# Kernel optimization log

Hardware: AMD Instinct MI355X
Metric: run time of the kernel (lower is better)

## Reference

```python
import jax, jax.numpy as jnp
import numpy as np

L, B = 64, 7          # n_layers, n_bit_options
EPS = 0.02            # sinkhorn entropic regularizer
ITERS = 200           # sinkhorn iterations
TINY = 1e-40


def setup_inputs() -> dict:
    key = jax.random.key(0)
    k1, k2, k3, k4 = jax.random.split(key, 4)
    theta = jax.random.normal(k1, (L, B), dtype=jnp.float32)
    phi = jax.random.normal(k2, (B,), dtype=jnp.float32)
    # layer sizes (param counts), positive; matches layer_sizes buffer usage
    n = jax.random.uniform(k3, (L,), dtype=jnp.float32, minval=4096.0, maxval=262144.0)
    sens = jax.random.uniform(k4, (L,), dtype=jnp.float32)
    sens = sens / sens.sum()  # update_sensitivity normalizes to a distribution
    bits = jnp.arange(2, 2 + B, dtype=jnp.float32)
    err = 2.0 ** (-2.0 * bits)  # quantization error per bitwidth
    return {"theta": theta, "phi": phi, "n": n, "sens": sens, "err": err}


def reference(theta, phi, n, sens, err):
    # DiffAllocator.compute_P
    a = n / n.sum()                         # row marginal (buffer 'a')
    b = jax.nn.softmax(phi)                 # col marginal b()
    C = (n * sens)[:, None] * err[None, :]  # build_cost: [L,B]
    K = -(C - theta) / EPS                  # log-kernel
    log_a = jnp.log(a + TINY)
    log_b = jnp.log(b + TINY)
    f0 = jnp.zeros((L,), dtype=theta.dtype)
    g0 = jnp.zeros((B,), dtype=theta.dtype)

    def step(carry, _):
        f, g = carry
        f = log_a - jax.scipy.special.logsumexp(K + g[None, :], axis=1)
        g = log_b - jax.scipy.special.logsumexp(K + f[:, None], axis=0)
        return (f, g), None

    (f, g), _ = jax.lax.scan(step, (f0, g0), None, length=ITERS)
    P = jnp.exp(K + f[:, None] + g[None, :])
    return P / (P.sum() + TINY)
```

## Files before the change

kernel.cpp:

```cpp
#include <hip/hip_runtime.h>
#include <math.h>

#define NB 7
#define EPS_ 0.02f
#define ITERS1_ 120
#define ITERS2_ 80
#define TINY_ 1e-40f
#define LOG2E_ 1.4426950408889634f
#define LN2_   0.6931471805599453f

__device__ __forceinline__ float exp2_hw(float x) {
#if __has_builtin(__builtin_amdgcn_exp2f)
    return __builtin_amdgcn_exp2f(x);
#else
    return __expf(x * LN2_);
#endif
}
__device__ __forceinline__ float log2_hw(float x) {
#if __has_builtin(__builtin_amdgcn_logf)
    return __builtin_amdgcn_logf(x);
#else
    return __logf(x) * LOG2E_;
#endif
}
__device__ __forceinline__ float rcp_hw(float x) {
#if __has_builtin(__builtin_amdgcn_rcpf)
    return __builtin_amdgcn_rcpf(x);
#else
    return 1.0f / x;
#endif
}

template <int CTRL>
__device__ __forceinline__ float dpp_ident(float identity, float x) {
    return __int_as_float(__builtin_amdgcn_update_dpp(
        __float_as_int(identity), __float_as_int(x), CTRL, 0xF, 0xF, false));
}
__device__ __forceinline__ float readlane63(float x) {
    return __int_as_float(__builtin_amdgcn_readlane(__float_as_int(x), 63));
}
__device__ __forceinline__ float wave_sum_bcast(float s) {
    s += dpp_ident<0x111>(0.f, s);
    s += dpp_ident<0x112>(0.f, s);
    s += dpp_ident<0x114>(0.f, s);
    s += dpp_ident<0x118>(0.f, s);
    s += dpp_ident<0x142>(0.f, s);
    s += dpp_ident<0x143>(0.f, s);
    return readlane63(s);
}

#define WAVE_MAX7(v0,v1,v2,v3,v4,v5,v6, m0,m1,m2,m3,m4,m5,m6)                 \
  {                                                                           \
    float r0,r1,r2,r3,r4,r5,r6;                                               \
    asm("v_mov_b32 %0, %14\n\t"                                               \
        "v_mov_b32 %1, %15\n\t"                                               \
        "v_mov_b32 %2, %16\n\t"                                               \
        "v_mov_b32 %3, %17\n\t"                                               \
        "v_mov_b32 %4, %18\n\t"                                               \
        "v_mov_b32 %5, %19\n\t"                                               \
        "v_mov_b32 %6, %20\n\t"                                               \
        "v_max_f32_dpp %0, %0, %0 row_shr:1 row_mask:0xf bank_mask:0xf\n\t"   \
        "v_max_f32_dpp %1, %1, %1 row_shr:1 row_mask:0xf bank_mask:0xf\n\t"   \
        "v_max_f32_dpp %2, %2, %2 row_shr:1 row_mask:0xf bank_mask:0xf\n\t"   \
        "v_max_f32_dpp %3, %3, %3 row_shr:1 row_mask:0xf bank_mask:0xf\n\t"   \
        "v_max_f32_dpp %4, %4, %4 row_shr:1 row_mask:0xf bank_mask:0xf\n\t"   \
        "v_max_f32_dpp %5, %5, %5 row_shr:1 row_mask:0xf bank_mask:0xf\n\t"   \
        "v_max_f32_dpp %6, %6, %6 row_shr:1 row_mask:0xf bank_mask:0xf\n\t"   \
        "v_max_f32_dpp %0, %0, %0 row_shr:2 row_mask:0xf bank_mask:0xf\n\t"   \
        "v_max_f32_dpp %1, %1, %1 row_shr:2 row_mask:0xf bank_mask:0xf\n\t"   \
        "v_max_f32_dpp %2, %2, %2 row_shr:2 row_mask:0xf bank_mask:0xf\n\t"   \
        "v_max_f32_dpp %3, %3, %3 row_shr:2 row_mask:0xf bank_mask:0xf\n\t"   \
        "v_max_f32_dpp %4, %4, %4 row_shr:2 row_mask:0xf bank_mask:0xf\n\t"   \
        "v_max_f32_dpp %5, %5, %5 row_shr:2 row_mask:0xf bank_mask:0xf\n\t"   \
        "v_max_f32_dpp %6, %6, %6 row_shr:2 row_mask:0xf bank_mask:0xf\n\t"   \
        "v_max_f32_dpp %0, %0, %0 row_shr:4 row_mask:0xf bank_mask:0xf\n\t"   \
        "v_max_f32_dpp %1, %1, %1 row_shr:4 row_mask:0xf bank_mask:0xf\n\t"   \
        "v_max_f32_dpp %2, %2, %2 row_shr:4 row_mask:0xf bank_mask:0xf\n\t"   \
        "v_max_f32_dpp %3, %3, %3 row_shr:4 row_mask:0xf bank_mask:0xf\n\t"   \
        "v_max_f32_dpp %4, %4, %4 row_shr:4 row_mask:0xf bank_mask:0xf\n\t"   \
        "v_max_f32_dpp %5, %5, %5 row_shr:4 row_mask:0xf bank_mask:0xf\n\t"   \
        "v_max_f32_dpp %6, %6, %6 row_shr:4 row_mask:0xf bank_mask:0xf\n\t"   \
        "v_max_f32_dpp %0, %0, %0 row_shr:8 row_mask:0xf bank_mask:0xf\n\t"   \
        "v_max_f32_dpp %1, %1, %1 row_shr:8 row_mask:0xf bank_mask:0xf\n\t"   \
        "v_max_f32_dpp %2, %2, %2 row_shr:8 row_mask:0xf bank_mask:0xf\n\t"   \
        "v_max_f32_dpp %3, %3, %3 row_shr:8 row_mask:0xf bank_mask:0xf\n\t"   \
        "v_max_f32_dpp %4, %4, %4 row_shr:8 row_mask:0xf bank_mask:0xf\n\t"   \
        "v_max_f32_dpp %5, %5, %5 row_shr:8 row_mask:0xf bank_mask:0xf\n\t"   \
        "v_max_f32_dpp %6, %6, %6 row_shr:8 row_mask:0xf bank_mask:0xf\n\t"   \
        "v_max_f32_dpp %0, %0, %0 row_bcast:15 row_mask:0xa bank_mask:0xf\n\t"\
        "v_max_f32_dpp %1, %1, %1 row_bcast:15 row_mask:0xa bank_mask:0xf\n\t"\
        "v_max_f32_dpp %2, %2, %2 row_bcast:15 row_mask:0xa bank_mask:0xf\n\t"\
        "v_max_f32_dpp %3, %3, %3 row_bcast:15 row_mask:0xa bank_mask:0xf\n\t"\
        "v_max_f32_dpp %4, %4, %4 row_bcast:15 row_mask:0xa bank_mask:0xf\n\t"\
        "v_max_f32_dpp %5, %5, %5 row_bcast:15 row_mask:0xa bank_mask:0xf\n\t"\
        "v_max_f32_dpp %6, %6, %6 row_bcast:15 row_mask:0xa bank_mask:0xf\n\t"\
        "v_max_f32_dpp %0, %0, %0 row_bcast:31 row_mask:0xc bank_mask:0xf\n\t"\
        "v_max_f32_dpp %1, %1, %1 row_bcast:31 row_mask:0xc bank_mask:0xf\n\t"\
        "v_max_f32_dpp %2, %2, %2 row_bcast:31 row_mask:0xc bank_mask:0xf\n\t"\
        "v_max_f32_dpp %3, %3, %3 row_bcast:31 row_mask:0xc bank_mask:0xf\n\t"\
        "v_max_f32_dpp %4, %4, %4 row_bcast:31 row_mask:0xc bank_mask:0xf\n\t"\
        "v_max_f32_dpp %5, %5, %5 row_bcast:31 row_mask:0xc bank_mask:0xf\n\t"\
        "v_max_f32_dpp %6, %6, %6 row_bcast:31 row_mask:0xc bank_mask:0xf\n\t"\
        "v_readlane_b32 %7, %0, 63\n\t"                                       \
        "v_readlane_b32 %8, %1, 63\n\t"                                       \
        "v_readlane_b32 %9, %2, 63\n\t"                                       \
        "v_readlane_b32 %10, %3, 63\n\t"                                      \
        "v_readlane_b32 %11, %4, 63\n\t"                                      \
        "v_readlane_b32 %12, %5, 63\n\t"                                      \
        "v_readlane_b32 %13, %6, 63\n\t"                                      \
        "s_nop 1"                                                             \
        : "=&v"(r0), "=&v"(r1), "=&v"(r2), "=&v"(r3),                         \
          "=&v"(r4), "=&v"(r5), "=&v"(r6),                                    \
          "=s"(m0), "=s"(m1), "=s"(m2), "=s"(m3),                             \
          "=s"(m4), "=s"(m5), "=s"(m6)                                        \
        : "v"(v0), "v"(v1), "v"(v2), "v"(v3), "v"(v4), "v"(v5), "v"(v6));     \
  }

#define WAVE_SUM7(e0,e1,e2,e3,e4,e5,e6, s0_,s1_,s2_,s3_,s4_,s5_,s6_)          \
    asm("s_nop 1\n\t"                                                         \
        "v_add_f32_dpp %0, %0, %0 row_shr:1 row_mask:0xf bank_mask:0xf\n\t"   \
        "v_add_f32_dpp %1, %1, %1 row_shr:1 row_mask:0xf bank_mask:0xf\n\t"   \
        "v_add_f32_dpp %2, %2, %2 row_shr:1 row_mask:0xf bank_mask:0xf\n\t"   \
        "v_add_f32_dpp %3, %3, %3 row_shr:1 row_mask:0xf bank_mask:0xf\n\t"   \
        "v_add_f32_dpp %4, %4, %4 row_shr:1 row_mask:0xf bank_mask:0xf\n\t"   \
        "v_add_f32_dpp %5, %5, %5 row_shr:1 row_mask:0xf bank_mask:0xf\n\t"   \
        "v_add_f32_dpp %6, %6, %6 row_shr:1 row_mask:0xf bank_mask:0xf\n\t"   \
        "v_add_f32_dpp %0, %0, %0 row_shr:2 row_mask:0xf bank_mask:0xf\n\t"   \
        "v_add_f32_dpp %1, %1, %1 row_shr:2 row_mask:0xf bank_mask:0xf\n\t"   \
        "v_add_f32_dpp %2, %2, %2 row_shr:2 row_mask:0xf bank_mask:0xf\n\t"   \
        "v_add_f32_dpp %3, %3, %3 row_shr:2 row_mask:0xf bank_mask:0xf\n\t"   \
        "v_add_f32_dpp %4, %4, %4 row_shr:2 row_mask:0xf bank_mask:0xf\n\t"   \
        "v_add_f32_dpp %5, %5, %5 row_shr:2 row_mask:0xf bank_mask:0xf\n\t"   \
        "v_add_f32_dpp %6, %6, %6 row_shr:2 row_mask:0xf bank_mask:0xf\n\t"   \
        "v_add_f32_dpp %0, %0, %0 row_shr:4 row_mask:0xf bank_mask:0xf\n\t"   \
        "v_add_f32_dpp %1, %1, %1 row_shr:4 row_mask:0xf bank_mask:0xf\n\t"   \
        "v_add_f32_dpp %2, %2, %2 row_shr:4 row_mask:0xf bank_mask:0xf\n\t"   \
        "v_add_f32_dpp %3, %3, %3 row_shr:4 row_mask:0xf bank_mask:0xf\n\t"   \
        "v_add_f32_dpp %4, %4, %4 row_shr:4 row_mask:0xf bank_mask:0xf\n\t"   \
        "v_add_f32_dpp %5, %5, %5 row_shr:4 row_mask:0xf bank_mask:0xf\n\t"   \
        "v_add_f32_dpp %6, %6, %6 row_shr:4 row_mask:0xf bank_mask:0xf\n\t"   \
        "v_add_f32_dpp %0, %0, %0 row_shr:8 row_mask:0xf bank_mask:0xf\n\t"   \
        "v_add_f32_dpp %1, %1, %1 row_shr:8 row_mask:0xf bank_mask:0xf\n\t"   \
        "v_add_f32_dpp %2, %2, %2 row_shr:8 row_mask:0xf bank_mask:0xf\n\t"   \
        "v_add_f32_dpp %3, %3, %3 row_shr:8 row_mask:0xf bank_mask:0xf\n\t"   \
        "v_add_f32_dpp %4, %4, %4 row_shr:8 row_mask:0xf bank_mask:0xf\n\t"   \
        "v_add_f32_dpp %5, %5, %5 row_shr:8 row_mask:0xf bank_mask:0xf\n\t"   \
        "v_add_f32_dpp %6, %6, %6 row_shr:8 row_mask:0xf bank_mask:0xf\n\t"   \
        "v_add_f32_dpp %0, %0, %0 row_bcast:15 row_mask:0xa bank_mask:0xf\n\t"\
        "v_add_f32_dpp %1, %1, %1 row_bcast:15 row_mask:0xa bank_mask:0xf\n\t"\
        "v_add_f32_dpp %2, %2, %2 row_bcast:15 row_mask:0xa bank_mask:0xf\n\t"\
        "v_add_f32_dpp %3, %3, %3 row_bcast:15 row_mask:0xa bank_mask:0xf\n\t"\
        "v_add_f32_dpp %4, %4, %4 row_bcast:15 row_mask:0xa bank_mask:0xf\n\t"\
        "v_add_f32_dpp %5, %5, %5 row_bcast:15 row_mask:0xa bank_mask:0xf\n\t"\
        "v_add_f32_dpp %6, %6, %6 row_bcast:15 row_mask:0xa bank_mask:0xf\n\t"\
        "v_add_f32_dpp %0, %0, %0 row_bcast:31 row_mask:0xc bank_mask:0xf\n\t"\
        "v_add_f32_dpp %1, %1, %1 row_bcast:31 row_mask:0xc bank_mask:0xf\n\t"\
        "v_add_f32_dpp %2, %2, %2 row_bcast:31 row_mask:0xc bank_mask:0xf\n\t"\
        "v_add_f32_dpp %3, %3, %3 row_bcast:31 row_mask:0xc bank_mask:0xf\n\t"\
        "v_add_f32_dpp %4, %4, %4 row_bcast:31 row_mask:0xc bank_mask:0xf\n\t"\
        "v_add_f32_dpp %5, %5, %5 row_bcast:31 row_mask:0xc bank_mask:0xf\n\t"\
        "v_add_f32_dpp %6, %6, %6 row_bcast:31 row_mask:0xc bank_mask:0xf\n\t"\
        "v_readlane_b32 %7, %0, 63\n\t"                                       \
        "v_readlane_b32 %8, %1, 63\n\t"                                       \
        "v_readlane_b32 %9, %2, 63\n\t"                                       \
        "v_readlane_b32 %10, %3, 63\n\t"                                      \
        "v_readlane_b32 %11, %4, 63\n\t"                                      \
        "v_readlane_b32 %12, %5, 63\n\t"                                      \
        "v_readlane_b32 %13, %6, 63\n\t"                                      \
        "s_nop 1"                                                             \
        : "+v"(e0), "+v"(e1), "+v"(e2), "+v"(e3),                             \
          "+v"(e4), "+v"(e5), "+v"(e6),                                       \
          "=s"(s0_), "=s"(s1_), "=s"(s2_), "=s"(s3_),                         \
          "=s"(s4_), "=s"(s5_), "=s"(s6_))

#define WAVE_SUM7_SRC(w0,w1,w2,w3,w4,w5,w6, s0_,s1_,s2_,s3_,s4_,s5_,s6_)     \
  {                                                                           \
    float r0,r1,r2,r3,r4,r5,r6;                                               \
    asm("s_nop 1\n\t"                                                         \
        "v_add_f32_dpp %0, %14, %14 row_shr:1 row_mask:0xf bank_mask:0xf\n\t" \
        "v_add_f32_dpp %1, %15, %15 row_shr:1 row_mask:0xf bank_mask:0xf\n\t" \
        "v_add_f32_dpp %2, %16, %16 row_shr:1 row_mask:0xf bank_mask:0xf\n\t" \
        "v_add_f32_dpp %3, %17, %17 row_shr:1 row_mask:0xf bank_mask:0xf\n\t" \
        "v_add_f32_dpp %4, %18, %18 row_shr:1 row_mask:0xf bank_mask:0xf\n\t" \
        "v_add_f32_dpp %5, %19, %19 row_shr:1 row_mask:0xf bank_mask:0xf\n\t" \
        "v_add_f32_dpp %6, %20, %20 row_shr:1 row_mask:0xf bank_mask:0xf\n\t" \
        "v_add_f32_dpp %0, %0, %0 row_shr:2 row_mask:0xf bank_mask:0xf\n\t"   \
        "v_add_f32_dpp %1, %1, %1 row_shr:2 row_mask:0xf bank_mask:0xf\n\t"   \
        "v_add_f32_dpp %2, %2, %2 row_shr:2 row_mask:0xf bank_mask:0xf\n\t"   \
        "v_add_f32_dpp %3, %3, %3 row_shr:2 row_mask:0xf bank_mask:0xf\n\t"   \
        "v_add_f32_dpp %4, %4, %4 row_shr:2 row_mask:0xf bank_mask:0xf\n\t"   \
        "v_add_f32_dpp %5, %5, %5 row_shr:2 row_mask:0xf bank_mask:0xf\n\t"   \
        "v_add_f32_dpp %6, %6, %6 row_shr:2 row_mask:0xf bank_mask:0xf\n\t"   \
        "v_add_f32_dpp %0, %0, %0 row_shr:4 row_mask:0xf bank_mask:0xf\n\t"   \
        "v_add_f32_dpp %1, %1, %1 row_shr:4 row_mask:0xf bank_mask:0xf\n\t"   \
        "v_add_f32_dpp %2, %2, %2 row_shr:4 row_mask:0xf bank_mask:0xf\n\t"   \
        "v_add_f32_dpp %3, %3, %3 row_shr:4 row_mask:0xf bank_mask:0xf\n\t"   \
        "v_add_f32_dpp %4, %4, %4 row_shr:4 row_mask:0xf bank_mask:0xf\n\t"   \
        "v_add_f32_dpp %5, %5, %5 row_shr:4 row_mask:0xf bank_mask:0xf\n\t"   \
        "v_add_f32_dpp %6, %6, %6 row_shr:4 row_mask:0xf bank_mask:0xf\n\t"   \
        "v_add_f32_dpp %0, %0, %0 row_shr:8 row_mask:0xf bank_mask:0xf\n\t"   \
        "v_add_f32_dpp %1, %1, %1 row_shr:8 row_mask:0xf bank_mask:0xf\n\t"   \
        "v_add_f32_dpp %2, %2, %2 row_shr:8 row_mask:0xf bank_mask:0xf\n\t"   \
        "v_add_f32_dpp %3, %3, %3 row_shr:8 row_mask:0xf bank_mask:0xf\n\t"   \
        "v_add_f32_dpp %4, %4, %4 row_shr:8 row_mask:0xf bank_mask:0xf\n\t"   \
        "v_add_f32_dpp %5, %5, %5 row_shr:8 row_mask:0xf bank_mask:0xf\n\t"   \
        "v_add_f32_dpp %6, %6, %6 row_shr:8 row_mask:0xf bank_mask:0xf\n\t"   \
        "v_add_f32_dpp %0, %0, %0 row_bcast:15 row_mask:0xa bank_mask:0xf\n\t"\
        "v_add_f32_dpp %1, %1, %1 row_bcast:15 row_mask:0xa bank_mask:0xf\n\t"\
        "v_add_f32_dpp %2, %2, %2 row_bcast:15 row_mask:0xa bank_mask:0xf\n\t"\
        "v_add_f32_dpp %3, %3, %3 row_bcast:15 row_mask:0xa bank_mask:0xf\n\t"\
        "v_add_f32_dpp %4, %4, %4 row_bcast:15 row_mask:0xa bank_mask:0xf\n\t"\
        "v_add_f32_dpp %5, %5, %5 row_bcast:15 row_mask:0xa bank_mask:0xf\n\t"\
        "v_add_f32_dpp %6, %6, %6 row_bcast:15 row_mask:0xa bank_mask:0xf\n\t"\
        "v_add_f32_dpp %0, %0, %0 row_bcast:31 row_mask:0xc bank_mask:0xf\n\t"\
        "v_add_f32_dpp %1, %1, %1 row_bcast:31 row_mask:0xc bank_mask:0xf\n\t"\
        "v_add_f32_dpp %2, %2, %2 row_bcast:31 row_mask:0xc bank_mask:0xf\n\t"\
        "v_add_f32_dpp %3, %3, %3 row_bcast:31 row_mask:0xc bank_mask:0xf\n\t"\
        "v_add_f32_dpp %4, %4, %4 row_bcast:31 row_mask:0xc bank_mask:0xf\n\t"\
        "v_add_f32_dpp %5, %5, %5 row_bcast:31 row_mask:0xc bank_mask:0xf\n\t"\
        "v_add_f32_dpp %6, %6, %6 row_bcast:31 row_mask:0xc bank_mask:0xf\n\t"\
        "v_readlane_b32 %7, %0, 63\n\t"                                       \
        "v_readlane_b32 %8, %1, 63\n\t"                                       \
        "v_readlane_b32 %9, %2, 63\n\t"                                       \
        "v_readlane_b32 %10, %3, 63\n\t"                                      \
        "v_readlane_b32 %11, %4, 63\n\t"                                      \
        "v_readlane_b32 %12, %5, 63\n\t"                                      \
        "v_readlane_b32 %13, %6, 63\n\t"                                      \
        "s_nop 1"                                                             \
        : "=&v"(r0), "=&v"(r1), "=&v"(r2), "=&v"(r3),                         \
          "=&v"(r4), "=&v"(r5), "=&v"(r6),                                    \
          "=s"(s0_), "=s"(s1_), "=s"(s2_), "=s"(s3_),                         \
          "=s"(s4_), "=s"(s5_), "=s"(s6_)                                     \
        : "v"(w0), "v"(w1), "v"(w2), "v"(w3), "v"(w4), "v"(w5), "v"(w6));     \
  }

__global__ __launch_bounds__(64) void sinkhorn_kernel(
    const float* __restrict__ theta,
    const float* __restrict__ phi,
    const float* __restrict__ n,
    const float* __restrict__ sens,
    const float* __restrict__ err,
    float* __restrict__ out)
{
    const int lane = threadIdx.x;

    const float ni = n[lane];
    const float si = sens[lane];

    const float kscale = LOG2E_ / EPS_;
    float K2[NB];
    #pragma unroll
    for (int j = 0; j < NB; ++j)
        K2[j] = (theta[lane * NB + j] - ni * si * err[j]) * kscale;

    const float nsum   = wave_sum_bcast(ni);
    const float aT     = ni / nsum + TINY_;
    const float log_a2 = log2_hw(aT);

    float t2v[NB];
    #pragma unroll
    for (int j = 0; j < NB; ++j) t2v[j] = phi[j] * LOG2E_;
    float pmax = t2v[0];
    #pragma unroll
    for (int j = 1; j < NB; ++j) pmax = fmaxf(pmax, t2v[j]);
    float psum = 0.f;
    #pragma unroll
    for (int j = 0; j < NB; ++j) psum += exp2_hw(t2v[j] - pmax);
    const float lps = log2_hw(psum);
    float bT[NB], log_b2[NB], cb[NB];
    #pragma unroll
    for (int j = 0; j < NB; ++j) {
        bT[j]     = exp2_hw(t2v[j] - pmax - lps) + TINY_;
        log_b2[j] = log2_hw(bT[j]);
        cb[j]     = log_b2[j] - log_a2;
    }

    float t[NB];
    #pragma unroll
    for (int j = 0; j < NB; ++j) t[j] = K2[j] - log_b2[j];

    const float LOF = __int_as_float(0x0D800000);
    const float HIF = __int_as_float(0x71800000);
    const unsigned LO = 0x0D800000u, HI = 0x71800000u;

    for (int it = 0; it < ITERS1_; ++it) {
        float a0 = t[0] + cb[0], a1 = t[1] + cb[1], a2 = t[2] + cb[2],
              a3 = t[3] + cb[3], a4 = t[4] + cb[4], a5 = t[5] + cb[5],
              a6 = t[6] + cb[6];
        float s = ((exp2_hw(a0) + exp2_hw(a1)) + (exp2_hw(a2) + exp2_hw(a3)))
                + ((exp2_hw(a4) + exp2_hw(a5)) + exp2_hw(a6));
        float L;
        const bool ok = (s >= LOF) && (s <= HIF);
        if (__ballot(ok) == ~0ull) {
            L = log2_hw(s);
        } else {
            float m = fmaxf(fmaxf(fmaxf(a0, a1), fmaxf(a2, a3)),
                            fmaxf(fmaxf(a4, a5), a6));
            float s2 = ((exp2_hw(a0 - m) + exp2_hw(a1 - m))
                      + (exp2_hw(a2 - m) + exp2_hw(a3 - m)))
                     + ((exp2_hw(a4 - m) + exp2_hw(a5 - m)) + exp2_hw(a6 - m));
            L = m + log2_hw(s2);
        }

        float q0 = t[0] - L, q1 = t[1] - L, q2 = t[2] - L, q3 = t[3] - L,
              q4 = t[4] - L, q5 = t[5] - L, q6 = t[6] - L;
        float e0 = exp2_hw(q0), e1 = exp2_hw(q1), e2 = exp2_hw(q2),
              e3 = exp2_hw(q3), e4 = exp2_hw(q4), e5 = exp2_hw(q5),
              e6 = exp2_hw(q6);
        float ss0, ss1, ss2, ss3, ss4, ss5, ss6;
        WAVE_SUM7(e0, e1, e2, e3, e4, e5, e6, ss0, ss1, ss2, ss3, ss4, ss5, ss6);

        const unsigned u0 = __float_as_uint(ss0), u1 = __float_as_uint(ss1),
                       u2 = __float_as_uint(ss2), u3 = __float_as_uint(ss3),
                       u4 = __float_as_uint(ss4), u5 = __float_as_uint(ss5),
                       u6 = __float_as_uint(ss6);
        const unsigned umin = min(min(min(u0, u1), min(u2, u3)),
                                  min(min(u4, u5), u6));
        const unsigned umax = max(max(max(u0, u1), max(u2, u3)),
                                  max(max(u4, u5), u6));
        if (umin < LO || umax > HI) {
            float M0, M1, M2, M3, M4, M5, M6;
            WAVE_MAX7(q0, q1, q2, q3, q4, q5, q6, M0, M1, M2, M3, M4, M5, M6);
            e0 = exp2_hw(q0 - M0); e1 = exp2_hw(q1 - M1);
            e2 = exp2_hw(q2 - M2); e3 = exp2_hw(q3 - M3);
            e4 = exp2_hw(q4 - M4); e5 = exp2_hw(q5 - M5);
            e6 = exp2_hw(q6 - M6);
            WAVE_SUM7(e0, e1, e2, e3, e4, e5, e6, ss0, ss1, ss2, ss3, ss4, ss5, ss6);
            t[0] = q0 - (M0 + log2_hw(ss0)); t[1] = q1 - (M1 + log2_hw(ss1));
            t[2] = q2 - (M2 + log2_hw(ss2)); t[3] = q3 - (M3 + log2_hw(ss3));
            t[4] = q4 - (M4 + log2_hw(ss4)); t[5] = q5 - (M5 + log2_hw(ss5));
            t[6] = q6 - (M6 + log2_hw(ss6));
        } else {
            t[0] = q0 - log2_hw(ss0); t[1] = q1 - log2_hw(ss1);
            t[2] = q2 - log2_hw(ss2); t[3] = q3 - log2_hw(ss3);
            t[4] = q4 - log2_hw(ss4); t[5] = q5 - log2_hw(ss5);
            t[6] = q6 - log2_hw(ss6);
        }
    }

    float U[NB], B[NB];
    #pragma unroll
    for (int j = 0; j < NB; ++j) {
        U[j] = exp2_hw(t[j]);
        B[j] = exp2_hw(cb[j]);
    }

    for (int it = 0; it < ITERS2_; ++it) {
        float p0 = U[0] * B[0], p1 = U[1] * B[1], p2 = U[2] * B[2],
              p3 = U[3] * B[3], p4 = U[4] * B[4], p5 = U[5] * B[5],
              p6 = U[6] * B[6];
        const float s = ((p0 + p1) + (p2 + p3)) + ((p4 + p5) + p6);
        const float rs = rcp_hw(s);
        float w0 = U[0] * rs, w1 = U[1] * rs, w2 = U[2] * rs,
              w3 = U[3] * rs, w4 = U[4] * rs, w5 = U[5] * rs,
              w6 = U[6] * rs;

        float ss0, ss1, ss2, ss3, ss4, ss5, ss6;
        WAVE_SUM7_SRC(w0, w1, w2, w3, w4, w5, w6,
                      ss0, ss1, ss2, ss3, ss4, ss5, ss6);

        const float r0 = rcp_hw(ss0);
        const float r1 = rcp_hw(ss1);
        const float r2 = rcp_hw(ss2);
        const float r3 = rcp_hw(ss3);
        const float r4 = rcp_hw(ss4);
        const float r5 = rcp_hw(ss5);
        const float r6 = rcp_hw(ss6);
        U[0] = w0 * r0; U[1] = w1 * r1; U[2] = w2 * r2; U[3] = w3 * r3;
        U[4] = w4 * r4; U[5] = w5 * r5; U[6] = w6 * r6;
    }

    float pr[NB];
    float rowsum = 0.f;
    #pragma unroll
    for (int j = 0; j < NB; ++j) {
        pr[j] = U[j] * bT[j];
        rowsum += pr[j];
    }
    const float total = wave_sum_bcast(rowsum);
    const float inv = 1.0f / (total + TINY_);
    #pragma unroll
    for (int j = 0; j < NB; ++j)
        out[lane * NB + j] = pr[j] * inv;
}

extern "C" void kernel_launch(void* const* d_in, const int* in_sizes, int n_in,
                              void* d_out, int out_size, void* d_ws, size_t ws_size,
                              hipStream_t stream) {
    const float* theta = (const float*)d_in[0];
    const float* phi   = (const float*)d_in[1];
    const float* n     = (const float*)d_in[2];
    const float* sens  = (const float*)d_in[3];
    const float* err   = (const float*)d_in[4];
    float* out = (float*)d_out;

    sinkhorn_kernel<<<1, 64, 0, stream>>>(theta, phi, n, sens, err, out);
}
```

Baseline: 115.2 us.

## Split Sinkhorn columns across seven waves with LDS row exchange

Launches seven wavefronts, one per bit-width column, so each lane holds a single element instead of seven. Column logsumexp and normalization use one wave-level DPP reduction per wave. Row reductions go through double-buffered shared memory with a block barrier each iteration. This shortens the per-wave instruction stream but adds LDS traffic and a __syncthreads on the serial critical path of every iteration.

```diff
diff --git a/kernel.cpp b/kernel.cpp
--- a/kernel.cpp
+++ b/kernel.cpp
@@ -48,193 +48,20 @@
     s += dpp_ident<0x143>(0.f, s);
     return readlane63(s);
 }
+__device__ __forceinline__ float wave_max_bcast(float m) {
+    const float NI = __int_as_float(0xff800000);
+    m = fmaxf(m, dpp_ident<0x111>(NI, m));
+    m = fmaxf(m, dpp_ident<0x112>(NI, m));
+    m = fmaxf(m, dpp_ident<0x114>(NI, m));
+    m = fmaxf(m, dpp_ident<0x118>(NI, m));
+    m = fmaxf(m, dpp_ident<0x142>(NI, m));
+    m = fmaxf(m, dpp_ident<0x143>(NI, m));
+    return readlane63(m);
+}
 
-#define WAVE_MAX7(v0,v1,v2,v3,v4,v5,v6, m0,m1,m2,m3,m4,m5,m6)                 \
-  {                                                                           \
-    float r0,r1,r2,r3,r4,r5,r6;                                               \
-    asm("v_mov_b32 %0, %14\n\t"                                               \
-        "v_mov_b32 %1, %15\n\t"                                               \
-        "v_mov_b32 %2, %16\n\t"                                               \
-        "v_mov_b32 %3, %17\n\t"                                               \
-        "v_mov_b32 %4, %18\n\t"                                               \
-        "v_mov_b32 %5, %19\n\t"                                               \
-        "v_mov_b32 %6, %20\n\t"                                               \
-        "v_max_f32_dpp %0, %0, %0 row_shr:1 row_mask:0xf bank_mask:0xf\n\t"   \
-        "v_max_f32_dpp %1, %1, %1 row_shr:1 row_mask:0xf bank_mask:0xf\n\t"   \
-        "v_max_f32_dpp %2, %2, %2 row_shr:1 row_mask:0xf bank_mask:0xf\n\t"   \
-        "v_max_f32_dpp %3, %3, %3 row_shr:1 row_mask:0xf bank_mask:0xf\n\t"   \
-        "v_max_f32_dpp %4, %4, %4 row_shr:1 row_mask:0xf bank_mask:0xf\n\t"   \
-        "v_max_f32_dpp %5, %5, %5 row_shr:1 row_mask:0xf bank_mask:0xf\n\t"   \
-        "v_max_f32_dpp %6, %6, %6 row_shr:1 row_mask:0xf bank_mask:0xf\n\t"   \
-        "v_max_f32_dpp %0, %0, %0 row_shr:2 row_mask:0xf bank_mask:0xf\n\t"   \
-        "v_max_f32_dpp %1, %1, %1 row_shr:2 row_mask:0xf bank_mask:0xf\n\t"   \
-        "v_max_f32_dpp %2, %2, %2 row_shr:2 row_mask:0xf bank_mask:0xf\n\t"   \
-        "v_max_f32_dpp %3, %3, %3 row_shr:2 row_mask:0xf bank_mask:0xf\n\t"   \
-        "v_max_f32_dpp %4, %4, %4 row_shr:2 row_mask:0xf bank_mask:0xf\n\t"   \
-        "v_max_f32_dpp %5, %5, %5 row_shr:2 row_mask:0xf bank_mask:0xf\n\t"   \
-        "v_max_f32_dpp %6, %6, %6 row_shr:2 row_mask:0xf bank_mask:0xf\n\t"   \
-        "v_max_f32_dpp %0, %0, %0 row_shr:4 row_mask:0xf bank_mask:0xf\n\t"   \
-        "v_max_f32_dpp %1, %1, %1 row_shr:4 row_mask:0xf bank_mask:0xf\n\t"   \
-        "v_max_f32_dpp %2, %2, %2 row_shr:4 row_mask:0xf bank_mask:0xf\n\t"   \
-        "v_max_f32_dpp %3, %3, %3 row_shr:4 row_mask:0xf bank_mask:0xf\n\t"   \
-        "v_max_f32_dpp %4, %4, %4 row_shr:4 row_mask:0xf bank_mask:0xf\n\t"   \
-        "v_max_f32_dpp %5, %5, %5 row_shr:4 row_mask:0xf bank_mask:0xf\n\t"   \
-        "v_max_f32_dpp %6, %6, %6 row_shr:4 row_mask:0xf bank_mask:0xf\n\t"   \
-        "v_max_f32_dpp %0, %0, %0 row_shr:8 row_mask:0xf bank_mask:0xf\n\t"   \
-        "v_max_f32_dpp %1, %1, %1 row_shr:8 row_mask:0xf bank_mask:0xf\n\t"   \
-        "v_max_f32_dpp %2, %2, %2 row_shr:8 row_mask:0xf bank_mask:0xf\n\t"   \
-        "v_max_f32_dpp %3, %3, %3 row_shr:8 row_mask:0xf bank_mask:0xf\n\t"   \
-        "v_max_f32_dpp %4, %4, %4 row_shr:8 row_mask:0xf bank_mask:0xf\n\t"   \
-        "v_max_f32_dpp %5, %5, %5 row_shr:8 row_mask:0xf bank_mask:0xf\n\t"   \
-        "v_max_f32_dpp %6, %6, %6 row_shr:8 row_mask:0xf bank_mask:0xf\n\t"   \
-        "v_max_f32_dpp %0, %0, %0 row_bcast:15 row_mask:0xa bank_mask:0xf\n\t"\
-        "v_max_f32_dpp %1, %1, %1 row_bcast:15 row_mask:0xa bank_mask:0xf\n\t"\
-        "v_max_f32_dpp %2, %2, %2 row_bcast:15 row_mask:0xa bank_mask:0xf\n\t"\
-        "v_max_f32_dpp %3, %3, %3 row_bcast:15 row_mask:0xa bank_mask:0xf\n\t"\
-        "v_max_f32_dpp %4, %4, %4 row_bcast:15 row_mask:0xa bank_mask:0xf\n\t"\
-        "v_max_f32_dpp %5, %5, %5 row_bcast:15 row_mask:0xa bank_mask:0xf\n\t"\
-        "v_max_f32_dpp %6, %6, %6 row_bcast:15 row_mask:0xa bank_mask:0xf\n\t"\
-        "v_max_f32_dpp %0, %0, %0 row_bcast:31 row_mask:0xc bank_mask:0xf\n\t"\
-        "v_max_f32_dpp %1, %1, %1 row_bcast:31 row_mask:0xc bank_mask:0xf\n\t"\
-        "v_max_f32_dpp %2, %2, %2 row_bcast:31 row_mask:0xc bank_mask:0xf\n\t"\
-        "v_max_f32_dpp %3, %3, %3 row_bcast:31 row_mask:0xc bank_mask:0xf\n\t"\
-        "v_max_f32_dpp %4, %4, %4 row_bcast:31 row_mask:0xc bank_mask:0xf\n\t"\
-        "v_max_f32_dpp %5, %5, %5 row_bcast:31 row_mask:0xc bank_mask:0xf\n\t"\
-        "v_max_f32_dpp %6, %6, %6 row_bcast:31 row_mask:0xc bank_mask:0xf\n\t"\
-        "v_readlane_b32 %7, %0, 63\n\t"                                       \
-        "v_readlane_b32 %8, %1, 63\n\t"                                       \
-        "v_readlane_b32 %9, %2, 63\n\t"                                       \
-        "v_readlane_b32 %10, %3, 63\n\t"                                      \
-        "v_readlane_b32 %11, %4, 63\n\t"                                      \
-        "v_readlane_b32 %12, %5, 63\n\t"                                      \
-        "v_readlane_b32 %13, %6, 63\n\t"                                      \
-        "s_nop 1"                                                             \
-        : "=&v"(r0), "=&v"(r1), "=&v"(r2), "=&v"(r3),                         \
-          "=&v"(r4), "=&v"(r5), "=&v"(r6),                                    \
-          "=s"(m0), "=s"(m1), "=s"(m2), "=s"(m3),                             \
-          "=s"(m4), "=s"(m5), "=s"(m6)                                        \
-        : "v"(v0), "v"(v1), "v"(v2), "v"(v3), "v"(v4), "v"(v5), "v"(v6));     \
-  }
+#define STRIDE_ 9
 
-#define WAVE_SUM7(e0,e1,e2,e3,e4,e5,e6, s0_,s1_,s2_,s3_,s4_,s5_,s6_)          \
-    asm("s_nop 1\n\t"                                                         \
-        "v_add_f32_dpp %0, %0, %0 row_shr:1 row_mask:0xf bank_mask:0xf\n\t"   \
-        "v_add_f32_dpp %1, %1, %1 row_shr:1 row_mask:0xf bank_mask:0xf\n\t"   \
-        "v_add_f32_dpp %2, %2, %2 row_shr:1 row_mask:0xf bank_mask:0xf\n\t"   \
-        "v_add_f32_dpp %3, %3, %3 row_shr:1 row_mask:0xf bank_mask:0xf\n\t"   \
-        "v_add_f32_dpp %4, %4, %4 row_shr:1 row_mask:0xf bank_mask:0xf\n\t"   \
-        "v_add_f32_dpp %5, %5, %5 row_shr:1 row_mask:0xf bank_mask:0xf\n\t"   \
-        "v_add_f32_dpp %6, %6, %6 row_shr:1 row_mask:0xf bank_mask:0xf\n\t"   \
-        "v_add_f32_dpp %0, %0, %0 row_shr:2 row_mask:0xf bank_mask:0xf\n\t"   \
-        "v_add_f32_dpp %1, %1, %1 row_shr:2 row_mask:0xf bank_mask:0xf\n\t"   \
-        "v_add_f32_dpp %2, %2, %2 row_shr:2 row_mask:0xf bank_mask:0xf\n\t"   \
-        "v_add_f32_dpp %3, %3, %3 row_shr:2 row_mask:0xf bank_mask:0xf\n\t"   \
-        "v_add_f32_dpp %4, %4, %4 row_shr:2 row_mask:0xf bank_mask:0xf\n\t"   \
-        "v_add_f32_dpp %5, %5, %5 row_shr:2 row_mask:0xf bank_mask:0xf\n\t"   \
-        "v_add_f32_dpp %6, %6, %6 row_shr:2 row_mask:0xf bank_mask:0xf\n\t"   \
-        "v_add_f32_dpp %0, %0, %0 row_shr:4 row_mask:0xf bank_mask:0xf\n\t"   \
-        "v_add_f32_dpp %1, %1, %1 row_shr:4 row_mask:0xf bank_mask:0xf\n\t"   \
-        "v_add_f32_dpp %2, %2, %2 row_shr:4 row_mask:0xf bank_mask:0xf\n\t"   \
-        "v_add_f32_dpp %3, %3, %3 row_shr:4 row_mask:0xf bank_mask:0xf\n\t"   \
-        "v_add_f32_dpp %4, %4, %4 row_shr:4 row_mask:0xf bank_mask:0xf\n\t"   \
-        "v_add_f32_dpp %5, %5, %5 row_shr:4 row_mask:0xf bank_mask:0xf\n\t"   \
-        "v_add_f32_dpp %6, %6, %6 row_shr:4 row_mask:0xf bank_mask:0xf\n\t"   \
-        "v_add_f32_dpp %0, %0, %0 row_shr:8 row_mask:0xf bank_mask:0xf\n\t"   \
-        "v_add_f32_dpp %1, %1, %1 row_shr:8 row_mask:0xf bank_mask:0xf\n\t"   \
-        "v_add_f32_dpp %2, %2, %2 row_shr:8 row_mask:0xf bank_mask:0xf\n\t"   \
-        "v_add_f32_dpp %3, %3, %3 row_shr:8 row_mask:0xf bank_mask:0xf\n\t"   \
-        "v_add_f32_dpp %4, %4, %4 row_shr:8 row_mask:0xf bank_mask:0xf\n\t"   \
-        "v_add_f32_dpp %5, %5, %5 row_shr:8 row_mask:0xf bank_mask:0xf\n\t"   \
-        "v_add_f32_dpp %6, %6, %6 row_shr:8 row_mask:0xf bank_mask:0xf\n\t"   \
-        "v_add_f32_dpp %0, %0, %0 row_bcast:15 row_mask:0xa bank_mask:0xf\n\t"\
-        "v_add_f32_dpp %1, %1, %1 row_bcast:15 row_mask:0xa bank_mask:0xf\n\t"\
-        "v_add_f32_dpp %2, %2, %2 row_bcast:15 row_mask:0xa bank_mask:0xf\n\t"\
-        "v_add_f32_dpp %3, %3, %3 row_bcast:15 row_mask:0xa bank_mask:0xf\n\t"\
-        "v_add_f32_dpp %4, %4, %4 row_bcast:15 row_mask:0xa bank_mask:0xf\n\t"\
-        "v_add_f32_dpp %5, %5, %5 row_bcast:15 row_mask:0xa bank_mask:0xf\n\t"\
-        "v_add_f32_dpp %6, %6, %6 row_bcast:15 row_mask:0xa bank_mask:0xf\n\t"\
-        "v_add_f32_dpp %0, %0, %0 row_bcast:31 row_mask:0xc bank_mask:0xf\n\t"\
-        "v_add_f32_dpp %1, %1, %1 row_bcast:31 row_mask:0xc bank_mask:0xf\n\t"\
-        "v_add_f32_dpp %2, %2, %2 row_bcast:31 row_mask:0xc bank_mask:0xf\n\t"\
-        "v_add_f32_dpp %3, %3, %3 row_bcast:31 row_mask:0xc bank_mask:0xf\n\t"\
-        "v_add_f32_dpp %4, %4, %4 row_bcast:31 row_mask:0xc bank_mask:0xf\n\t"\
-        "v_add_f32_dpp %5, %5, %5 row_bcast:31 row_mask:0xc bank_mask:0xf\n\t"\
-        "v_add_f32_dpp %6, %6, %6 row_bcast:31 row_mask:0xc bank_mask:0xf\n\t"\
-        "v_readlane_b32 %7, %0, 63\n\t"                                       \
-        "v_readlane_b32 %8, %1, 63\n\t"                                       \
-        "v_readlane_b32 %9, %2, 63\n\t"                                       \
-        "v_readlane_b32 %10, %3, 63\n\t"                                      \
-        "v_readlane_b32 %11, %4, 63\n\t"                                      \
-        "v_readlane_b32 %12, %5, 63\n\t"                                      \
-        "v_readlane_b32 %13, %6, 63\n\t"                                      \
-        "s_nop 1"                                                             \
-        : "+v"(e0), "+v"(e1), "+v"(e2), "+v"(e3),                             \
-          "+v"(e4), "+v"(e5), "+v"(e6),                                       \
-          "=s"(s0_), "=s"(s1_), "=s"(s2_), "=s"(s3_),                         \
-          "=s"(s4_), "=s"(s5_), "=s"(s6_))
-
-#define WAVE_SUM7_SRC(w0,w1,w2,w3,w4,w5,w6, s0_,s1_,s2_,s3_,s4_,s5_,s6_)     \
-  {                                                                           \
-    float r0,r1,r2,r3,r4,r5,r6;                                               \
-    asm("s_nop 1\n\t"                                                         \
-        "v_add_f32_dpp %0, %14, %14 row_shr:1 row_mask:0xf bank_mask:0xf\n\t" \
-        "v_add_f32_dpp %1, %15, %15 row_shr:1 row_mask:0xf bank_mask:0xf\n\t" \
-        "v_add_f32_dpp %2, %16, %16 row_shr:1 row_mask:0xf bank_mask:0xf\n\t" \
-        "v_add_f32_dpp %3, %17, %17 row_shr:1 row_mask:0xf bank_mask:0xf\n\t" \
-        "v_add_f32_dpp %4, %18, %18 row_shr:1 row_mask:0xf bank_mask:0xf\n\t" \
-        "v_add_f32_dpp %5, %19, %19 row_shr:1 row_mask:0xf bank_mask:0xf\n\t" \
-        "v_add_f32_dpp %6, %20, %20 row_shr:1 row_mask:0xf bank_mask:0xf\n\t" \
-        "v_add_f32_dpp %0, %0, %0 row_shr:2 row_mask:0xf bank_mask:0xf\n\t"   \
-        "v_add_f32_dpp %1, %1, %1 row_shr:2 row_mask:0xf bank_mask:0xf\n\t"   \
-        "v_add_f32_dpp %2, %2, %2 row_shr:2 row_mask:0xf bank_mask:0xf\n\t"   \
-        "v_add_f32_dpp %3, %3, %3 row_shr:2 row_mask:0xf bank_mask:0xf\n\t"   \
-        "v_add_f32_dpp %4, %4, %4 row_shr:2 row_mask:0xf bank_mask:0xf\n\t"   \
-        "v_add_f32_dpp %5, %5, %5 row_shr:2 row_mask:0xf bank_mask:0xf\n\t"   \
-        "v_add_f32_dpp %6, %6, %6 row_shr:2 row_mask:0xf bank_mask:0xf\n\t"   \
-        "v_add_f32_dpp %0, %0, %0 row_shr:4 row_mask:0xf bank_mask:0xf\n\t"   \
-        "v_add_f32_dpp %1, %1, %1 row_shr:4 row_mask:0xf bank_mask:0xf\n\t"   \
-        "v_add_f32_dpp %2, %2, %2 row_shr:4 row_mask:0xf bank_mask:0xf\n\t"   \
-        "v_add_f32_dpp %3, %3, %3 row_shr:4 row_mask:0xf bank_mask:0xf\n\t"   \
-        "v_add_f32_dpp %4, %4, %4 row_shr:4 row_mask:0xf bank_mask:0xf\n\t"   \
-        "v_add_f32_dpp %5, %5, %5 row_shr:4 row_mask:0xf bank_mask:0xf\n\t"   \
-        "v_add_f32_dpp %6, %6, %6 row_shr:4 row_mask:0xf bank_mask:0xf\n\t"   \
-        "v_add_f32_dpp %0, %0, %0 row_shr:8 row_mask:0xf bank_mask:0xf\n\t"   \
-        "v_add_f32_dpp %1, %1, %1 row_shr:8 row_mask:0xf bank_mask:0xf\n\t"   \
-        "v_add_f32_dpp %2, %2, %2 row_shr:8 row_mask:0xf bank_mask:0xf\n\t"   \
-        "v_add_f32_dpp %3, %3, %3 row_shr:8 row_mask:0xf bank_mask:0xf\n\t"   \
-        "v_add_f32_dpp %4, %4, %4 row_shr:8 row_mask:0xf bank_mask:0xf\n\t"   \
-        "v_add_f32_dpp %5, %5, %5 row_shr:8 row_mask:0xf bank_mask:0xf\n\t"   \
-        "v_add_f32_dpp %6, %6, %6 row_shr:8 row_mask:0xf bank_mask:0xf\n\t"   \
-        "v_add_f32_dpp %0, %0, %0 row_bcast:15 row_mask:0xa bank_mask:0xf\n\t"\
-        "v_add_f32_dpp %1, %1, %1 row_bcast:15 row_mask:0xa bank_mask:0xf\n\t"\
-        "v_add_f32_dpp %2, %2, %2 row_bcast:15 row_mask:0xa bank_mask:0xf\n\t"\
-        "v_add_f32_dpp %3, %3, %3 row_bcast:15 row_mask:0xa bank_mask:0xf\n\t"\
-        "v_add_f32_dpp %4, %4, %4 row_bcast:15 row_mask:0xa bank_mask:0xf\n\t"\
-        "v_add_f32_dpp %5, %5, %5 row_bcast:15 row_mask:0xa bank_mask:0xf\n\t"\
-        "v_add_f32_dpp %6, %6, %6 row_bcast:15 row_mask:0xa bank_mask:0xf\n\t"\
-        "v_add_f32_dpp %0, %0, %0 row_bcast:31 row_mask:0xc bank_mask:0xf\n\t"\
-        "v_add_f32_dpp %1, %1, %1 row_bcast:31 row_mask:0xc bank_mask:0xf\n\t"\
-        "v_add_f32_dpp %2, %2, %2 row_bcast:31 row_mask:0xc bank_mask:0xf\n\t"\
-        "v_add_f32_dpp %3, %3, %3 row_bcast:31 row_mask:0xc bank_mask:0xf\n\t"\
-        "v_add_f32_dpp %4, %4, %4 row_bcast:31 row_mask:0xc bank_mask:0xf\n\t"\
-        "v_add_f32_dpp %5, %5, %5 row_bcast:31 row_mask:0xc bank_mask:0xf\n\t"\
-        "v_add_f32_dpp %6, %6, %6 row_bcast:31 row_mask:0xc bank_mask:0xf\n\t"\
-        "v_readlane_b32 %7, %0, 63\n\t"                                       \
-        "v_readlane_b32 %8, %1, 63\n\t"                                       \
-        "v_readlane_b32 %9, %2, 63\n\t"                                       \
-        "v_readlane_b32 %10, %3, 63\n\t"                                      \
-        "v_readlane_b32 %11, %4, 63\n\t"                                      \
-        "v_readlane_b32 %12, %5, 63\n\t"                                      \
-        "v_readlane_b32 %13, %6, 63\n\t"                                      \
-        "s_nop 1"                                                             \
-        : "=&v"(r0), "=&v"(r1), "=&v"(r2), "=&v"(r3),                         \
-          "=&v"(r4), "=&v"(r5), "=&v"(r6),                                    \
-          "=s"(s0_), "=s"(s1_), "=s"(s2_), "=s"(s3_),                         \
-          "=s"(s4_), "=s"(s5_), "=s"(s6_)                                     \
-        : "v"(w0), "v"(w1), "v"(w2), "v"(w3), "v"(w4), "v"(w5), "v"(w6));     \
-  }
-
-__global__ __launch_bounds__(64) void sinkhorn_kernel(
+__global__ __launch_bounds__(448) void sinkhorn_kernel(
     const float* __restrict__ theta,
     const float* __restrict__ phi,
     const float* __restrict__ n,
@@ -242,146 +69,117 @@
     const float* __restrict__ err,
     float* __restrict__ out)
 {
-    const int lane = threadIdx.x;
+    const int tid  = threadIdx.x;
+    const int lane = tid & 63;
+    const int wid  = tid >> 6;
+
+    __shared__ float bufEA[2][64 * STRIDE_ + 8];
+    __shared__ float bufAA[2][64 * STRIDE_ + 8];
+    __shared__ float ldsS[8];
 
     const float ni = n[lane];
     const float si = sens[lane];
-
-    const float kscale = LOG2E_ / EPS_;
-    float K2[NB];
-    #pragma unroll
-    for (int j = 0; j < NB; ++j)
-        K2[j] = (theta[lane * NB + j] - ni * si * err[j]) * kscale;
+    const float ej = err[wid];
+    const float th = theta[lane * NB + wid];
 
     const float nsum   = wave_sum_bcast(ni);
     const float aT     = ni / nsum + TINY_;
     const float log_a2 = log2_hw(aT);
 
-    float t2v[NB];
-    #pragma unroll
-    for (int j = 0; j < NB; ++j) t2v[j] = phi[j] * LOG2E_;
-    float pmax = t2v[0];
-    #pragma unroll
-    for (int j = 1; j < NB; ++j) pmax = fmaxf(pmax, t2v[j]);
-    float psum = 0.f;
-    #pragma unroll
-    for (int j = 0; j < NB; ++j) psum += exp2_hw(t2v[j] - pmax);
-    const float lps = log2_hw(psum);
-    float bT[NB], log_b2[NB], cb[NB];
-    #pragma unroll
-    for (int j = 0; j < NB; ++j) {
-        bT[j]     = exp2_hw(t2v[j] - pmax - lps) + TINY_;
-        log_b2[j] = log2_hw(bT[j]);
-        cb[j]     = log_b2[j] - log_a2;
-    }
+    float t2v0 = phi[0] * LOG2E_, t2v1 = phi[1] * LOG2E_,
+          t2v2 = phi[2] * LOG2E_, t2v3 = phi[3] * LOG2E_,
+          t2v4 = phi[4] * LOG2E_, t2v5 = phi[5] * LOG2E_,
+          t2v6 = phi[6] * LOG2E_;
+    float pmax = t2v0;
+    pmax = fmaxf(pmax, t2v1); pmax = fmaxf(pmax, t2v2);
+    pmax = fmaxf(pmax, t2v3); pmax = fmaxf(pmax, t2v4);
+    pmax = fmaxf(pmax, t2v5); pmax = fmaxf(pmax, t2v6);
+    float psum = exp2_hw(t2v0 - pmax);
+    psum += exp2_hw(t2v1 - pmax); psum += exp2_hw(t2v2 - pmax);
+    psum += exp2_hw(t2v3 - pmax); psum += exp2_hw(t2v4 - pmax);
+    psum += exp2_hw(t2v5 - pmax); psum += exp2_hw(t2v6 - pmax);
+    const float lps  = log2_hw(psum);
+    const float myt2 = phi[wid] * LOG2E_;
+    const float bTj  = exp2_hw(myt2 - pmax - lps) + TINY_;
+    const float lb2j = log2_hw(bTj);
+    const float cbj  = lb2j - log_a2;
 
-    float t[NB];
-    #pragma unroll
-    for (int j = 0; j < NB; ++j) t[j] = K2[j] - log_b2[j];
+    const float kscale = LOG2E_ / EPS_;
+    float t = (th - ni * si * ej) * kscale - lb2j;
 
     const float LOF = __int_as_float(0x0D800000);
     const float HIF = __int_as_float(0x71800000);
-    const unsigned LO = 0x0D800000u, HI = 0x71800000u;
+    const int   base = lane * STRIDE_ + wid;
+    const int   rb   = lane * STRIDE_;
 
     for (int it = 0; it < ITERS1_; ++it) {
-        float a0 = t[0] + cb[0], a1 = t[1] + cb[1], a2 = t[2] + cb[2],
-              a3 = t[3] + cb[3], a4 = t[4] + cb[4], a5 = t[5] + cb[5],
-              a6 = t[6] + cb[6];
-        float s = ((exp2_hw(a0) + exp2_hw(a1)) + (exp2_hw(a2) + exp2_hw(a3)))
-                + ((exp2_hw(a4) + exp2_hw(a5)) + exp2_hw(a6));
+        const int p = it & 1;
+        const float a = t + cbj;
+        bufEA[p][base] = exp2_hw(a);
+        bufAA[p][base] = a;
+        __syncthreads();
+
+        const float e0 = bufEA[p][rb + 0], e1 = bufEA[p][rb + 1],
+                    e2 = bufEA[p][rb + 2], e3 = bufEA[p][rb + 3],
+                    e4 = bufEA[p][rb + 4], e5 = bufEA[p][rb + 5],
+                    e6 = bufEA[p][rb + 6];
+        const float s = ((e0 + e1) + (e2 + e3)) + ((e4 + e5) + e6);
         float L;
         const bool ok = (s >= LOF) && (s <= HIF);
         if (__ballot(ok) == ~0ull) {
             L = log2_hw(s);
         } else {
-            float m = fmaxf(fmaxf(fmaxf(a0, a1), fmaxf(a2, a3)),
-                            fmaxf(fmaxf(a4, a5), a6));
-            float s2 = ((exp2_hw(a0 - m) + exp2_hw(a1 - m))
-                      + (exp2_hw(a2 - m) + exp2_hw(a3 - m)))
-                     + ((exp2_hw(a4 - m) + exp2_hw(a5 - m)) + exp2_hw(a6 - m));
+            const float a0 = bufAA[p][rb + 0], a1 = bufAA[p][rb + 1],
+                        a2 = bufAA[p][rb + 2], a3 = bufAA[p][rb + 3],
+                        a4 = bufAA[p][rb + 4], a5 = bufAA[p][rb + 5],
+                        a6 = bufAA[p][rb + 6];
+            const float m = fmaxf(fmaxf(fmaxf(a0, a1), fmaxf(a2, a3)),
+                                  fmaxf(fmaxf(a4, a5), a6));
+            const float s2 = ((exp2_hw(a0 - m) + exp2_hw(a1 - m))
+                            + (exp2_hw(a2 - m) + exp2_hw(a3 - m)))
+                           + ((exp2_hw(a4 - m) + exp2_hw(a5 - m))
+                            + exp2_hw(a6 - m));
             L = m + log2_hw(s2);
         }
 
-        float q0 = t[0] - L, q1 = t[1] - L, q2 = t[2] - L, q3 = t[3] - L,
-              q4 = t[4] - L, q5 = t[5] - L, q6 = t[6] - L;
-        float e0 = exp2_hw(q0), e1 = exp2_hw(q1), e2 = exp2_hw(q2),
-              e3 = exp2_hw(q3), e4 = exp2_hw(q4), e5 = exp2_hw(q5),
-              e6 = exp2_hw(q6);
-        float ss0, ss1, ss2, ss3, ss4, ss5, ss6;
-        WAVE_SUM7(e0, e1, e2, e3, e4, e5, e6, ss0, ss1, ss2, ss3, ss4, ss5, ss6);
-
-        const unsigned u0 = __float_as_uint(ss0), u1 = __float_as_uint(ss1),
-                       u2 = __float_as_uint(ss2), u3 = __float_as_uint(ss3),
-                       u4 = __float_as_uint(ss4), u5 = __float_as_uint(ss5),
-                       u6 = __float_as_uint(ss6);
-        const unsigned umin = min(min(min(u0, u1), min(u2, u3)),
-                                  min(min(u4, u5), u6));
-        const unsigned umax = max(max(max(u0, u1), max(u2, u3)),
-                                  max(max(u4, u5), u6));
-        if (umin < LO || umax > HI) {
-            float M0, M1, M2, M3, M4, M5, M6;
-            WAVE_MAX7(q0, q1, q2, q3, q4, q5, q6, M0, M1, M2, M3, M4, M5, M6);
-            e0 = exp2_hw(q0 - M0); e1 = exp2_hw(q1 - M1);
-            e2 = exp2_hw(q2 - M2); e3 = exp2_hw(q3 - M3);
-            e4 = exp2_hw(q4 - M4); e5 = exp2_hw(q5 - M5);
-            e6 = exp2_hw(q6 - M6);
-            WAVE_SUM7(e0, e1, e2, e3, e4, e5, e6, ss0, ss1, ss2, ss3, ss4, ss5, ss6);
-            t[0] = q0 - (M0 + log2_hw(ss0)); t[1] = q1 - (M1 + log2_hw(ss1));
-            t[2] = q2 - (M2 + log2_hw(ss2)); t[3] = q3 - (M3 + log2_hw(ss3));
-            t[4] = q4 - (M4 + log2_hw(ss4)); t[5] = q5 - (M5 + log2_hw(ss5));
-            t[6] = q6 - (M6 + log2_hw(ss6));
+        const float q = t - L;
+        const float e = exp2_hw(q);
+        const float ss = wave_sum_bcast(e);
+        if (ss >= LOF && ss <= HIF) {
+            t = q - log2_hw(ss);
         } else {
-            t[0] = q0 - log2_hw(ss0); t[1] = q1 - log2_hw(ss1);
-            t[2] = q2 - log2_hw(ss2); t[3] = q3 - log2_hw(ss3);
-            t[4] = q4 - log2_hw(ss4); t[5] = q5 - log2_hw(ss5);
-            t[6] = q6 - log2_hw(ss6);
+            const float M   = wave_max_bcast(q);
+            const float e2  = exp2_hw(q - M);
+            const float ss2 = wave_sum_bcast(e2);
+            t = q - (M + log2_hw(ss2));
         }
     }
 
-    float U[NB], B[NB];
-    #pragma unroll
-    for (int j = 0; j < NB; ++j) {
-        U[j] = exp2_hw(t[j]);
-        B[j] = exp2_hw(cb[j]);
+    float U = exp2_hw(t);
+    const float Bj = exp2_hw(cbj);
+
+    for (int it2 = 0; it2 < ITERS2_; ++it2) {
+        const int p = it2 & 1;
+        bufEA[p][base] = U * Bj;
+        __syncthreads();
+        const float p0 = bufEA[p][rb + 0], p1 = bufEA[p][rb + 1],
+                    p2 = bufEA[p][rb + 2], p3 = bufEA[p][rb + 3],
+                    p4 = bufEA[p][rb + 4], p5 = bufEA[p][rb + 5],
+                    p6 = bufEA[p][rb + 6];
+        const float s  = ((p0 + p1) + (p2 + p3)) + ((p4 + p5) + p6);
+        const float rs = rcp_hw(s);
+        const float w  = U * rs;
+        const float ss = wave_sum_bcast(w);
+        U = w * rcp_hw(ss);
     }
 
-    for (int it = 0; it < ITERS2_; ++it) {
-        float p0 = U[0] * B[0], p1 = U[1] * B[1], p2 = U[2] * B[2],
-              p3 = U[3] * B[3], p4 = U[4] * B[4], p5 = U[5] * B[5],
-              p6 = U[6] * B[6];
-        const float s = ((p0 + p1) + (p2 + p3)) + ((p4 + p5) + p6);
-        const float rs = rcp_hw(s);
-        float w0 = U[0] * rs, w1 = U[1] * rs, w2 = U[2] * rs,
-              w3 = U[3] * rs, w4 = U[4] * rs, w5 = U[5] * rs,
-              w6 = U[6] * rs;
-
-        float ss0, ss1, ss2, ss3, ss4, ss5, ss6;
-        WAVE_SUM7_SRC(w0, w1, w2, w3, w4, w5, w6,
-                      ss0, ss1, ss2, ss3, ss4, ss5, ss6);
-
-        const float r0 = rcp_hw(ss0);
-        const float r1 = rcp_hw(ss1);
-        const float r2 = rcp_hw(ss2);
-        const float r3 = rcp_hw(ss3);
-        const float r4 = rcp_hw(ss4);
-        const float r5 = rcp_hw(ss5);
-        const float r6 = rcp_hw(ss6);
-        U[0] = w0 * r0; U[1] = w1 * r1; U[2] = w2 * r2; U[3] = w3 * r3;
-        U[4] = w4 * r4; U[5] = w5 * r5; U[6] = w6 * r6;
-    }
-
-    float pr[NB];
-    float rowsum = 0.f;
-    #pragma unroll
-    for (int j = 0; j < NB; ++j) {
-        pr[j] = U[j] * bT[j];
-        rowsum += pr[j];
-    }
-    const float total = wave_sum_bcast(rowsum);
-    const float inv = 1.0f / (total + TINY_);
-    #pragma unroll
-    for (int j = 0; j < NB; ++j)
-        out[lane * NB + j] = pr[j] * inv;
+    const float pr = U * bTj;
+    const float cs = wave_sum_bcast(pr);
+    if (lane == 0) ldsS[wid] = cs;
+    __syncthreads();
+    const float total = ((ldsS[0] + ldsS[1]) + (ldsS[2] + ldsS[3]))
+                      + ((ldsS[4] + ldsS[5]) + ldsS[6]);
+    out[lane * NB + wid] = pr * (1.0f / (total + TINY_));
 }
 
 extern "C" void kernel_launch(void* const* d_in, const int* in_sizes, int n_in,
@@ -394,5 +192,5 @@
     const float* err   = (const float*)d_in[4];
     float* out = (float*)d_out;
 
-    sinkhorn_kernel<<<1, 64, 0, stream>>>(theta, phi, n, sens, err, out);
+    sinkhorn_kernel<<<1, 448, 0, stream>>>(theta, phi, n, sens, err, out);
 }
```

Result: faster. 111.3 us (-3.4%).
